# Kernel tuning notes

Measured on AMD Instinct MI355X. Metric: run time of the kernel, lower is better.

The kernel has to match this reference:

```python
import jax, jax.numpy as jnp
import numpy as np

EMB = 300
HID = 1024
RELU = 512
NCLS = 3
T = 8192


def _lstm_layer(x, Wih, Whh, bih, bhh):
    # x: [T, in_dim]; PyTorch gate order i, f, g, o; batch = 1 so state is a vector.
    H = Whh.shape[1]
    xg = x @ Wih.T + bih  # [T, 4H], input projection hoisted out of the scan

    def step(carry, xg_t):
        h, c = carry
        gates = xg_t + Whh @ h + bhh
        i, f, g, o = jnp.split(gates, 4)
        i = jax.nn.sigmoid(i)
        f = jax.nn.sigmoid(f)
        g = jnp.tanh(g)
        o = jax.nn.sigmoid(o)
        c = f * c + i * g
        h = o * jnp.tanh(c)
        return (h, c), h

    h0 = jnp.zeros((H,), x.dtype)
    (_, _), hs = jax.lax.scan(step, (h0, h0), xg)
    return hs  # [T, H]


def setup_inputs() -> dict:
    key = jax.random.key(0)
    ks = jax.random.split(key, 16)
    s_lstm = 1.0 / np.sqrt(HID)

    def n(k, shape, s):
        return (jax.random.normal(k, shape, dtype=jnp.float32) * s)

    return {
        "quote": n(ks[0], (T, EMB), 1.0),
        "Wih0": n(ks[1], (4 * HID, EMB), s_lstm),
        "Whh0": n(ks[2], (4 * HID, HID), s_lstm),
        "bih0": n(ks[3], (4 * HID,), s_lstm),
        "bhh0": n(ks[4], (4 * HID,), s_lstm),
        "Wih1": n(ks[5], (4 * HID, HID), s_lstm),
        "Whh1": n(ks[6], (4 * HID, HID), s_lstm),
        "bih1": n(ks[7], (4 * HID,), s_lstm),
        "bhh1": n(ks[8], (4 * HID,), s_lstm),
        "W0": n(ks[9], (RELU, HID), 1.0 / np.sqrt(HID)),
        "b0": n(ks[10], (RELU,), 0.01),
        "W1": n(ks[11], (RELU, RELU), 1.0 / np.sqrt(RELU)),
        "b1": n(ks[12], (RELU,), 0.01),
        "W2": n(ks[13], (NCLS, RELU), 1.0 / np.sqrt(RELU)),
        "b2": n(ks[14], (NCLS,), 0.01),
    }


def reference(quote, Wih0, Whh0, bih0, bhh0, Wih1, Whh1, bih1, bhh1,
              W0, b0, W1, b1, W2, b2):
    h1 = _lstm_layer(quote, Wih0, Whh0, bih0, bhh0)  # [T, HID]
    h2 = _lstm_layer(h1, Wih1, Whh1, bih1, bhh1)     # [T, HID]
    last = h2[-1]                                     # lstmOut of final word, batch 1
    x = jax.nn.relu(last @ W0.T + b0)
    x = jax.nn.relu(x @ W1.T + b1)
    # Dropout(p=0.5) is identity in eval mode.
    logits = (x @ W2.T + b2).reshape(1, NCLS)
    return jax.nn.log_softmax(logits, axis=1)
```

## Files before the change

kernel.cpp:

```cpp
#include <hip/hip_runtime.h>
#include <stdint.h>

typedef unsigned int uint32;
typedef unsigned long long uint64;

#define T_SEQ 8192

#define WO_WHH0  0ull
#define WO_WIH0  8388608ull
#define WO_WHH1  10878976ull
#define WO_WIH1  19267584ull
#define WO_B0    27656192ull
#define WO_B1    27672576ull
#define WO_H1    27688960ull
#define WO_H2    27697152ull
#define WO_CST0  27705344ull
#define WO_CST1  27709440ull
#define WO_Y0    27713536ull
#define WO_Y1    27715584ull

__device__ __forceinline__ float bflo(uint32 u){ return __uint_as_float(u << 16); }
__device__ __forceinline__ float bfhi(uint32 u){ return __uint_as_float(u & 0xffff0000u); }

__device__ __forceinline__ unsigned short f2bf(float f){
  uint32 u = __float_as_uint(f);
  u += 0x7fffu + ((u >> 16) & 1u);
  return (unsigned short)(u >> 16);
}

__device__ __forceinline__ void mac8(float& a, uint4 w,
    float h0,float h1,float h2,float h3,float h4,float h5,float h6,float h7){
  a = fmaf(bflo(w.x), h0, a); a = fmaf(bfhi(w.x), h1, a);
  a = fmaf(bflo(w.y), h2, a); a = fmaf(bfhi(w.y), h3, a);
  a = fmaf(bflo(w.z), h4, a); a = fmaf(bfhi(w.z), h5, a);
  a = fmaf(bflo(w.w), h6, a); a = fmaf(bfhi(w.w), h7, a);
}

extern "C" __global__ void __launch_bounds__(256)
prep_weights(const float* __restrict__ Wih0, const float* __restrict__ Whh0,
             const float* __restrict__ bih0, const float* __restrict__ bhh0,
             const float* __restrict__ Wih1, const float* __restrict__ Whh1,
             const float* __restrict__ bih1, const float* __restrict__ bhh1,
             char* __restrict__ ws)
{
  unsigned short* whh0b = (unsigned short*)(ws + WO_WHH0);
  unsigned short* wih0b = (unsigned short*)(ws + WO_WIH0);
  unsigned short* whh1b = (unsigned short*)(ws + WO_WHH1);
  unsigned short* wih1b = (unsigned short*)(ws + WO_WIH1);
  float* b0 = (float*)(ws + WO_B0);
  float* b1 = (float*)(ws + WO_B1);

  const int stride = gridDim.x * blockDim.x;
  const int tid0 = blockIdx.x * blockDim.x + threadIdx.x;

  for (int i = tid0; i < 4096*1024; i += stride) whh0b[i] = f2bf(Whh0[i]);
  for (int i = tid0; i < 4096*1024; i += stride) whh1b[i] = f2bf(Whh1[i]);
  for (int i = tid0; i < 4096*1024; i += stride) wih1b[i] = f2bf(Wih1[i]);
  for (int i = tid0; i < 4096*304;  i += stride) {
    int r = i / 304, x = i - r * 304;
    wih0b[i] = f2bf(x < 300 ? Wih0[(size_t)r * 300 + x] : 0.0f);
  }
  for (int i = tid0; i < 4096; i += stride) {
    b0[i] = bih0[i] + bhh0[i];
    b1[i] = bih1[i] + bhh1[i];
  }
}

extern "C" __global__ void __launch_bounds__(256)
lstm_step(int t, const float* __restrict__ quote, char* __restrict__ ws)
{
  const unsigned short* whh0b = (const unsigned short*)(ws + WO_WHH0);
  const unsigned short* wih0b = (const unsigned short*)(ws + WO_WIH0);
  const unsigned short* whh1b = (const unsigned short*)(ws + WO_WHH1);
  const unsigned short* wih1b = (const unsigned short*)(ws + WO_WIH1);
  const float* b0 = (const float*)(ws + WO_B0);
  const float* b1 = (const float*)(ws + WO_B1);
  float* h1buf = (float*)(ws + WO_H1);
  float* h2buf = (float*)(ws + WO_H2);
  float* cst0  = (float*)(ws + WO_CST0);
  float* cst1  = (float*)(ws + WO_CST1);

  const int tid = threadIdx.x;
  const int wv  = tid >> 6;
  const int c   = tid & 63;

  float acc[4];
  #pragma unroll
  for (int i = 0; i < 4; ++i) acc[i] = 0.0f;

  if (blockIdx.x < 256) {
    if (t >= T_SEQ) return;
    const int u = (int)blockIdx.x * 4 + wv;

    float hv[16];
    if (t > 0) {
      const float4* hb4 = (const float4*)(h1buf + (size_t)((t - 1) & 1) * 1024 + (c << 4));
      float4 a0 = hb4[0], a1 = hb4[1], a2 = hb4[2], a3 = hb4[3];
      hv[0]=a0.x; hv[1]=a0.y; hv[2]=a0.z; hv[3]=a0.w;
      hv[4]=a1.x; hv[5]=a1.y; hv[6]=a1.z; hv[7]=a1.w;
      hv[8]=a2.x; hv[9]=a2.y; hv[10]=a2.z; hv[11]=a2.w;
      hv[12]=a3.x; hv[13]=a3.y; hv[14]=a3.z; hv[15]=a3.w;
    }
    if (c < 38) {
      float xv[8];
      int x0 = c << 3;
      const float* xr = quote + (size_t)t * 300;
      #pragma unroll
      for (int m = 0; m < 8; ++m) xv[m] = (x0 + m < 300) ? xr[x0 + m] : 0.0f;
      #pragma unroll
      for (int g = 0; g < 4; ++g) {
        int row = (g << 10) + u;
        uint4 w = *(const uint4*)(wih0b + (size_t)row * 304 + (c << 3));
        mac8(acc[g], w, xv[0],xv[1],xv[2],xv[3],xv[4],xv[5],xv[6],xv[7]);
      }
    }
    if (t > 0) {
      #pragma unroll
      for (int g = 0; g < 4; ++g) {
        int row = (g << 10) + u;
        const uint4* wp = (const uint4*)(whh0b + (size_t)row * 1024 + (c << 4));
        uint4 w0 = wp[0], w1 = wp[1];
        mac8(acc[g], w0, hv[0],hv[1],hv[2],hv[3],hv[4],hv[5],hv[6],hv[7]);
        mac8(acc[g], w1, hv[8],hv[9],hv[10],hv[11],hv[12],hv[13],hv[14],hv[15]);
      }
    }
    #pragma unroll
    for (int i = 0; i < 4; ++i) {
      #pragma unroll
      for (int m = 1; m < 64; m <<= 1) acc[i] += __shfl_xor(acc[i], m);
    }
    if (c == 0) {
      float pre[4];
      #pragma unroll
      for (int g = 0; g < 4; ++g) pre[g] = acc[g] + b0[(g << 10) + u];
      float ig = 1.0f/(1.0f+expf(-pre[0])), fg = 1.0f/(1.0f+expf(-pre[1]));
      float gg = tanhf(pre[2]),             og = 1.0f/(1.0f+expf(-pre[3]));
      float cs = fg * cst0[u] + ig * gg;
      cst0[u] = cs;
      h1buf[(size_t)(t & 1) * 1024 + u] = og * tanhf(cs);
    }
  } else {
    __shared__ float sred[16];
    const int s = t - 1;
    if (s < 0) return;
    const int lb = (int)blockIdx.x - 256;
    const int u  = lb * 2 + (wv >> 1);
    const int mtx = wv & 1;

    const bool active = (mtx == 0) || (s > 0);
    if (active) {
      const float* hsrc = (mtx == 0) ? (h1buf + (size_t)(s & 1) * 1024)
                                     : (h2buf + (size_t)((s - 1) & 1) * 1024);
      const unsigned short* wb = (mtx == 0) ? wih1b : whh1b;
      const float4* hb4 = (const float4*)(hsrc + (c << 4));
      float4 a0 = hb4[0], a1 = hb4[1], a2 = hb4[2], a3 = hb4[3];
      float hv[16] = {a0.x,a0.y,a0.z,a0.w, a1.x,a1.y,a1.z,a1.w,
                      a2.x,a2.y,a2.z,a2.w, a3.x,a3.y,a3.z,a3.w};
      #pragma unroll
      for (int g = 0; g < 4; ++g) {
        int row = (g << 10) + u;
        const uint4* wp = (const uint4*)(wb + (size_t)row * 1024 + (c << 4));
        uint4 w0 = wp[0], w1 = wp[1];
        mac8(acc[g], w0, hv[0],hv[1],hv[2],hv[3],hv[4],hv[5],hv[6],hv[7]);
        mac8(acc[g], w1, hv[8],hv[9],hv[10],hv[11],hv[12],hv[13],hv[14],hv[15]);
      }
    }
    #pragma unroll
    for (int i = 0; i < 4; ++i) {
      #pragma unroll
      for (int m = 1; m < 64; m <<= 1) acc[i] += __shfl_xor(acc[i], m);
    }
    if (c == 0) {
      #pragma unroll
      for (int g = 0; g < 4; ++g) sred[wv * 4 + g] = acc[g];
    }
    __syncthreads();
    if (mtx == 0 && c == 0) {
      float pre[4];
      #pragma unroll
      for (int g = 0; g < 4; ++g)
        pre[g] = acc[g] + sred[(wv + 1) * 4 + g] + b1[(g << 10) + u];
      float ig = 1.0f/(1.0f+expf(-pre[0])), fg = 1.0f/(1.0f+expf(-pre[1]));
      float gg = tanhf(pre[2]),             og = 1.0f/(1.0f+expf(-pre[3]));
      float cs = fg * cst1[u] + ig * gg;
      cst1[u] = cs;
      h2buf[(size_t)(s & 1) * 1024 + u] = og * tanhf(cs);
    }
  }
}

extern "C" __global__ void __launch_bounds__(256)
head_fc(const float* __restrict__ W, const float* __restrict__ b,
        const float* __restrict__ xin, float* __restrict__ y, int n_in)
{
  __shared__ float sred[256];
  const int i = blockIdx.x;
  float p = 0.0f;
  for (int k = threadIdx.x; k < n_in; k += 256)
    p = fmaf(W[(size_t)i * n_in + k], xin[k], p);
  sred[threadIdx.x] = p;
  __syncthreads();
  for (int s = 128; s > 0; s >>= 1) {
    if (threadIdx.x < s) sred[threadIdx.x] += sred[threadIdx.x + s];
    __syncthreads();
  }
  if (threadIdx.x == 0) y[i] = fmaxf(sred[0] + b[i], 0.0f);
}

extern "C" __global__ void __launch_bounds__(64)
head_out(const float* __restrict__ W2, const float* __restrict__ b2,
         const float* __restrict__ y1, float* __restrict__ out)
{
  const int l = threadIdx.x;
  float p0 = 0.0f, p1 = 0.0f, p2 = 0.0f;
  for (int k = l; k < 512; k += 64) {
    float v = y1[k];
    p0 = fmaf(W2[k],        v, p0);
    p1 = fmaf(W2[512 + k],  v, p1);
    p2 = fmaf(W2[1024 + k], v, p2);
  }
  #pragma unroll
  for (int m = 1; m < 64; m <<= 1) {
    p0 += __shfl_xor(p0, m);
    p1 += __shfl_xor(p1, m);
    p2 += __shfl_xor(p2, m);
  }
  if (l == 0) {
    float z0 = p0 + b2[0], z1 = p1 + b2[1], z2 = p2 + b2[2];
    float mx = fmaxf(z0, fmaxf(z1, z2));
    float lse = mx + logf(expf(z0 - mx) + expf(z1 - mx) + expf(z2 - mx));
    out[0] = z0 - lse; out[1] = z1 - lse; out[2] = z2 - lse;
  }
}

extern "C" void kernel_launch(void* const* d_in, const int* in_sizes, int n_in,
                              void* d_out, int out_size, void* d_ws, size_t ws_size,
                              hipStream_t stream)
{
  (void)in_sizes; (void)n_in; (void)out_size; (void)ws_size;
  const float* quote = (const float*)d_in[0];
  const float* Wih0  = (const float*)d_in[1];
  const float* Whh0  = (const float*)d_in[2];
  const float* bih0  = (const float*)d_in[3];
  const float* bhh0  = (const float*)d_in[4];
  const float* Wih1  = (const float*)d_in[5];
  const float* Whh1  = (const float*)d_in[6];
  const float* bih1  = (const float*)d_in[7];
  const float* bhh1  = (const float*)d_in[8];
  const float* W0    = (const float*)d_in[9];
  const float* b0    = (const float*)d_in[10];
  const float* W1    = (const float*)d_in[11];
  const float* b1    = (const float*)d_in[12];
  const float* W2    = (const float*)d_in[13];
  const float* b2    = (const float*)d_in[14];

  char* ws = (char*)d_ws;
  float* h2buf = (float*)(ws + WO_H2);
  float* y0    = (float*)(ws + WO_Y0);
  float* y1    = (float*)(ws + WO_Y1);

  hipMemsetAsync(ws + WO_CST0, 0, 8192, stream);

  prep_weights<<<2048, 256, 0, stream>>>(Wih0, Whh0, bih0, bhh0,
                                         Wih1, Whh1, bih1, bhh1, ws);

  for (int t = 0; t <= T_SEQ; ++t)
    lstm_step<<<768, 256, 0, stream>>>(t, quote, ws);

  head_fc<<<512, 256, 0, stream>>>(W0, b0, h2buf + 1024, y0, 1024);
  head_fc<<<512, 256, 0, stream>>>(W1, b1, y0, y1, 512);
  head_out<<<1, 64, 0, stream>>>(W2, b2, y1, (float*)d_out);
}
```

Before: 43.11 ms.

## Batch layer-1 input projection into chunked GEMMs with lagged second-layer recurrence

Layer-1 h outputs now go to a 512-entry ring buffer. Every 128 steps a separate kernel computes the Wih1 projection for that chunk of timesteps, reusing weights held in registers across the 128 steps. The second-layer recurrence runs DLAG steps behind layer 0 and reads the precomputed projections, so the per-step kernel drops from 768 to 512 blocks and no longer streams Wih1 every step. The cost is 132 extra step launches, 64 serialized GEMM launches, and a larger workspace.

```diff
diff --git a/kernel.cpp b/kernel.cpp
--- a/kernel.cpp
+++ b/kernel.cpp
@@ -5,6 +5,7 @@
 typedef unsigned long long uint64;
 
 #define T_SEQ 8192
+#define DLAG  132
 
 #define WO_WHH0  0ull
 #define WO_WIH0  8388608ull
@@ -12,12 +13,13 @@
 #define WO_WIH1  19267584ull
 #define WO_B0    27656192ull
 #define WO_B1    27672576ull
-#define WO_H1    27688960ull
-#define WO_H2    27697152ull
-#define WO_CST0  27705344ull
-#define WO_CST1  27709440ull
-#define WO_Y0    27713536ull
-#define WO_Y1    27715584ull
+#define WO_H1R   27688960ull
+#define WO_Z1R   29786112ull
+#define WO_H2    33980416ull
+#define WO_CST0  33988608ull
+#define WO_CST1  33992704ull
+#define WO_Y0    33996800ull
+#define WO_Y1    33998848ull
 
 __device__ __forceinline__ float bflo(uint32 u){ return __uint_as_float(u << 16); }
 __device__ __forceinline__ float bfhi(uint32 u){ return __uint_as_float(u & 0xffff0000u); }
@@ -67,15 +69,54 @@
 }
 
 extern "C" __global__ void __launch_bounds__(256)
+gemm_z1(int c, char* __restrict__ ws)
+{
+  const unsigned short* wih1b = (const unsigned short*)(ws + WO_WIH1);
+  const float* h1r = (const float*)(ws + WO_H1R);
+  float* z1r = (float*)(ws + WO_Z1R);
+
+  const int tid = threadIdx.x;
+  const int wv  = tid >> 6;
+  const int cc  = tid & 63;
+  const int row0 = (int)blockIdx.x * 8 + wv * 2;
+
+  const uint4* wpA = (const uint4*)(wih1b + (size_t)row0 * 1024 + (cc << 4));
+  const uint4* wpB = (const uint4*)(wih1b + (size_t)(row0 + 1) * 1024 + (cc << 4));
+  uint4 wA0 = wpA[0], wA1 = wpA[1];
+  uint4 wB0 = wpB[0], wB1 = wpB[1];
+
+  float* zbase = z1r + (size_t)(c & 1) * 524288;
+  for (int sl = 0; sl < 128; ++sl) {
+    const int s = c * 128 + sl;
+    const float4* hb4 = (const float4*)(h1r + (size_t)(s & 511) * 1024 + (cc << 4));
+    float4 a0 = hb4[0], a1 = hb4[1], a2 = hb4[2], a3 = hb4[3];
+    float aA = 0.0f, aB = 0.0f;
+    mac8(aA, wA0, a0.x,a0.y,a0.z,a0.w, a1.x,a1.y,a1.z,a1.w);
+    mac8(aA, wA1, a2.x,a2.y,a2.z,a2.w, a3.x,a3.y,a3.z,a3.w);
+    mac8(aB, wB0, a0.x,a0.y,a0.z,a0.w, a1.x,a1.y,a1.z,a1.w);
+    mac8(aB, wB1, a2.x,a2.y,a2.z,a2.w, a3.x,a3.y,a3.z,a3.w);
+    #pragma unroll
+    for (int m = 1; m < 64; m <<= 1) {
+      aA += __shfl_xor(aA, m);
+      aB += __shfl_xor(aB, m);
+    }
+    if (cc == 0) {
+      zbase[(size_t)sl * 4096 + row0]     = aA;
+      zbase[(size_t)sl * 4096 + row0 + 1] = aB;
+    }
+  }
+}
+
+extern "C" __global__ void __launch_bounds__(256)
 lstm_step(int t, const float* __restrict__ quote, char* __restrict__ ws)
 {
   const unsigned short* whh0b = (const unsigned short*)(ws + WO_WHH0);
   const unsigned short* wih0b = (const unsigned short*)(ws + WO_WIH0);
   const unsigned short* whh1b = (const unsigned short*)(ws + WO_WHH1);
-  const unsigned short* wih1b = (const unsigned short*)(ws + WO_WIH1);
   const float* b0 = (const float*)(ws + WO_B0);
   const float* b1 = (const float*)(ws + WO_B1);
-  float* h1buf = (float*)(ws + WO_H1);
+  float* h1r   = (float*)(ws + WO_H1R);
+  float* z1r   = (float*)(ws + WO_Z1R);
   float* h2buf = (float*)(ws + WO_H2);
   float* cst0  = (float*)(ws + WO_CST0);
   float* cst1  = (float*)(ws + WO_CST1);
@@ -94,7 +135,7 @@
 
     float hv[16];
     if (t > 0) {
-      const float4* hb4 = (const float4*)(h1buf + (size_t)((t - 1) & 1) * 1024 + (c << 4));
+      const float4* hb4 = (const float4*)(h1r + (size_t)((t - 1) & 511) * 1024 + (c << 4));
       float4 a0 = hb4[0], a1 = hb4[1], a2 = hb4[2], a3 = hb4[3];
       hv[0]=a0.x; hv[1]=a0.y; hv[2]=a0.z; hv[3]=a0.w;
       hv[4]=a1.x; hv[5]=a1.y; hv[6]=a1.z; hv[7]=a1.w;
@@ -137,29 +178,27 @@
       float gg = tanhf(pre[2]),             og = 1.0f/(1.0f+expf(-pre[3]));
       float cs = fg * cst0[u] + ig * gg;
       cst0[u] = cs;
-      h1buf[(size_t)(t & 1) * 1024 + u] = og * tanhf(cs);
+      h1r[(size_t)(t & 511) * 1024 + u] = og * tanhf(cs);
     }
   } else {
-    __shared__ float sred[16];
-    const int s = t - 1;
-    if (s < 0) return;
-    const int lb = (int)blockIdx.x - 256;
-    const int u  = lb * 2 + (wv >> 1);
-    const int mtx = wv & 1;
-
-    const bool active = (mtx == 0) || (s > 0);
-    if (active) {
-      const float* hsrc = (mtx == 0) ? (h1buf + (size_t)(s & 1) * 1024)
-                                     : (h2buf + (size_t)((s - 1) & 1) * 1024);
-      const unsigned short* wb = (mtx == 0) ? wih1b : whh1b;
-      const float4* hb4 = (const float4*)(hsrc + (c << 4));
+    const int s = t - DLAG;
+    if (s < 0 || s >= T_SEQ) return;
+    const int u = ((int)blockIdx.x - 256) * 4 + wv;
+
+    const float* zb = z1r + (size_t)((s >> 7) & 1) * 524288 + (size_t)(s & 127) * 4096;
+    float zv[4];
+    #pragma unroll
+    for (int g = 0; g < 4; ++g) zv[g] = zb[(g << 10) + u];
+
+    if (s > 0) {
+      const float4* hb4 = (const float4*)(h2buf + (size_t)((s - 1) & 1) * 1024 + (c << 4));
       float4 a0 = hb4[0], a1 = hb4[1], a2 = hb4[2], a3 = hb4[3];
       float hv[16] = {a0.x,a0.y,a0.z,a0.w, a1.x,a1.y,a1.z,a1.w,
                       a2.x,a2.y,a2.z,a2.w, a3.x,a3.y,a3.z,a3.w};
       #pragma unroll
       for (int g = 0; g < 4; ++g) {
         int row = (g << 10) + u;
-        const uint4* wp = (const uint4*)(wb + (size_t)row * 1024 + (c << 4));
+        const uint4* wp = (const uint4*)(whh1b + (size_t)row * 1024 + (c << 4));
         uint4 w0 = wp[0], w1 = wp[1];
         mac8(acc[g], w0, hv[0],hv[1],hv[2],hv[3],hv[4],hv[5],hv[6],hv[7]);
         mac8(acc[g], w1, hv[8],hv[9],hv[10],hv[11],hv[12],hv[13],hv[14],hv[15]);
@@ -171,15 +210,9 @@
       for (int m = 1; m < 64; m <<= 1) acc[i] += __shfl_xor(acc[i], m);
     }
     if (c == 0) {
-      #pragma unroll
-      for (int g = 0; g < 4; ++g) sred[wv * 4 + g] = acc[g];
-    }
-    __syncthreads();
-    if (mtx == 0 && c == 0) {
       float pre[4];
       #pragma unroll
-      for (int g = 0; g < 4; ++g)
-        pre[g] = acc[g] + sred[(wv + 1) * 4 + g] + b1[(g << 10) + u];
+      for (int g = 0; g < 4; ++g) pre[g] = acc[g] + zv[g] + b1[(g << 10) + u];
       float ig = 1.0f/(1.0f+expf(-pre[0])), fg = 1.0f/(1.0f+expf(-pre[1]));
       float gg = tanhf(pre[2]),             og = 1.0f/(1.0f+expf(-pre[3]));
       float cs = fg * cst1[u] + ig * gg;
@@ -264,8 +297,11 @@
   prep_weights<<<2048, 256, 0, stream>>>(Wih0, Whh0, bih0, bhh0,
                                          Wih1, Whh1, bih1, bhh1, ws);
 
-  for (int t = 0; t <= T_SEQ; ++t)
-    lstm_step<<<768, 256, 0, stream>>>(t, quote, ws);
+  for (int t = 0; t <= T_SEQ - 1 + DLAG; ++t) {
+    lstm_step<<<512, 256, 0, stream>>>(t, quote, ws);
+    if (t < T_SEQ && ((t + 1) & 127) == 0)
+      gemm_z1<<<512, 256, 0, stream>>>((t + 1) / 128 - 1, ws);
+  }
 
   head_fc<<<512, 256, 0, stream>>>(W0, b0, h2buf + 1024, y0, 1024);
   head_fc<<<512, 256, 0, stream>>>(W1, b1, y0, y1, 512);
```

Measured after the change: 48.93 ms. +13.5%, slower.
